# Optimization experiments

Measured on AMD Instinct MI355X. Metric: run time of the kernel, lower is better.

The kernel has to match this reference:

```python
import jax, jax.numpy as jnp
import numpy as np

N_SRC = 200_000
N_DST = 40_000
N_EDGES = 8_000_000
N_LAYERS = 6
TH_R = 0.4  # dR threshold for class_name == 'supercharged'


def delta_r(phi0, eta0, phi1, eta1):
    deta = eta0 - eta1
    dphi = phi0 - phi1
    pi = jnp.float32(np.pi)
    dphi = jnp.where(dphi > pi, dphi - 2 * pi, dphi)
    dphi = jnp.where(dphi < -pi, dphi + 2 * pi, dphi)
    return jnp.sqrt(deta ** 2 + dphi ** 2)


def setup_inputs() -> dict:
    key = jax.random.key(0)
    ks = jax.random.split(key, 8)
    src = jax.random.randint(ks[0], (N_EDGES,), 0, N_SRC, dtype=jnp.int32)
    dst = jax.random.randint(ks[1], (N_EDGES,), 0, N_DST, dtype=jnp.int32)
    energy = jax.random.uniform(ks[2], (N_SRC,), dtype=jnp.float32)
    layer = jax.random.randint(ks[3], (N_SRC,), 0, N_LAYERS, dtype=jnp.int32)
    eta_src = jax.random.normal(ks[4], (N_SRC,), dtype=jnp.float32)
    phi_src = jax.random.normal(ks[5], (N_SRC,), dtype=jnp.float32)
    eta_dst = jax.random.normal(ks[6], (N_DST,), dtype=jnp.float32)
    phi_dst = jax.random.normal(ks[7], (N_DST,), dtype=jnp.float32)
    return {"src": src, "dst": dst, "energy": energy, "layer": layer,
            "eta_src": eta_src, "phi_src": phi_src,
            "eta_dst": eta_dst, "phi_dst": phi_dst}


def reference(src, dst, energy, layer, eta_src, phi_src, eta_dst, phi_dst):
    # --- edge_function_dR_reco: per-edge gather + dR mask ---
    dR = delta_r(phi_src[src], eta_src[src], phi_dst[dst], eta_dst[dst])  # [E]
    edge_dR_labels = (dR < TH_R).astype(energy.dtype)                      # [E]

    # --- particle_message: 6 layer-bucketed masked energies per edge ---
    e = energy[src] * edge_dR_labels                                       # [E]
    onehot = (layer[src][:, None] == jnp.arange(N_LAYERS)[None, :])        # [E,6]
    msgs = e[:, None] * onehot.astype(e.dtype)                             # [E,6]

    # --- particle_update: ragged mailbox sum + sample std per dst node ---
    seg_sum = jax.ops.segment_sum(msgs, dst, num_segments=N_DST)           # [N_dst,6]
    seg_sq = jax.ops.segment_sum(msgs * msgs, dst, num_segments=N_DST)     # [N_dst,6]
    deg = jax.ops.segment_sum(jnp.ones_like(e), dst, num_segments=N_DST)   # [N_dst]
    deg = deg[:, None]

    valid = deg > 1
    mean = seg_sum / jnp.maximum(deg, 1.0)
    # unbiased sample variance, as in torch.std(dim=1)
    var = (seg_sq - deg * mean * mean) / jnp.maximum(deg - 1.0, 1.0)
    var = jnp.maximum(var, 0.0)
    safe = var > 0
    std = jnp.where(safe, jnp.sqrt(jnp.where(safe, var, 1.0)), 0.0)
    std = jnp.where(valid, std, 0.0)

    return jnp.concatenate([seg_sum, std], axis=1)  # [N_dst, 12]
```

## Files before the change

kernel.cpp:

```cpp
#include <hip/hip_runtime.h>
#include <math.h>

#define N_SRC 200000
#define N_DST 40000
#define N_EDGES 8000000
#define N_LAYERS 6

#define EBLK 256
#define ETPB 1024
#define PDST_LDS 12288

typedef int vint4 __attribute__((ext_vector_type(4)));

__device__ float4 g_psrc[N_SRC];
__device__ float2 g_pdst[N_DST];
__device__ unsigned int g_partial[EBLK][N_DST / 4];

__global__ __launch_bounds__(256) void pack_kernel(
        const float* __restrict__ energy, const int* __restrict__ layer,
        const float* __restrict__ eta_s, const float* __restrict__ phi_s,
        const float* __restrict__ eta_d, const float* __restrict__ phi_d) {
    int i = blockIdx.x * blockDim.x + threadIdx.x;
    if (i < N_SRC) {
        float4 p;
        p.x = energy[i];
        p.y = eta_s[i];
        p.z = phi_s[i];
        p.w = __int_as_float(layer[i]);
        g_psrc[i] = p;
    }
    if (i < N_DST) g_pdst[i] = make_float2(eta_d[i], phi_d[i]);
}

__device__ __forceinline__ void edge_compute(const float2* __restrict__ pcache,
                                             unsigned int* __restrict__ bins,
                                             int s, int d,
                                             float* __restrict__ out) {
    atomicAdd(&bins[d >> 2], 1u << ((d & 3) * 8));

    float4 p = g_psrc[s];
    float2 q;
    if (d < PDST_LDS) q = pcache[d];
    else              q = g_pdst[d];

    const float pif   = 3.14159265358979323846f;
    const float twopi = 6.28318530717958647692f;
    float deta = p.y - q.x;
    float dphi = p.z - q.y;
    dphi = (dphi >  pif) ? dphi - twopi : dphi;
    dphi = (dphi < -pif) ? dphi + twopi : dphi;
    float dr = sqrtf(deta * deta + dphi * dphi);
    if (dr < 0.4f) {
        int   l = __float_as_int(p.w);
        float e = p.x;
        float* base = out + (size_t)d * 12;
        atomicAdd(base + l,     e);
        atomicAdd(base + 6 + l, e * e);
    }
}

__global__ __launch_bounds__(ETPB) void edge_kernel(
        const vint4* __restrict__ src4, const vint4* __restrict__ dst4,
        float* __restrict__ out) {
    __shared__ unsigned int bins[N_DST / 4];
    __shared__ float2 pcache[PDST_LDS];

    for (int i = threadIdx.x; i < N_DST / 4; i += ETPB) bins[i] = 0u;
    for (int i = threadIdx.x; i < PDST_LDS; i += ETPB) pcache[i] = g_pdst[i];
    __syncthreads();

    const int nvec = N_EDGES / 4;
    for (int v = blockIdx.x * ETPB + threadIdx.x; v < nvec; v += EBLK * ETPB) {
        vint4 s4 = __builtin_nontemporal_load(src4 + v);
        vint4 d4 = __builtin_nontemporal_load(dst4 + v);
        edge_compute(pcache, bins, s4.x, d4.x, out);
        edge_compute(pcache, bins, s4.y, d4.y, out);
        edge_compute(pcache, bins, s4.z, d4.z, out);
        edge_compute(pcache, bins, s4.w, d4.w, out);
    }
    __syncthreads();

    unsigned int* po = &g_partial[blockIdx.x][0];
    for (int i = threadIdx.x; i < N_DST / 4; i += ETPB)
        __builtin_nontemporal_store(bins[i], po + i);
}

__device__ __forceinline__ void finalize_one(float* __restrict__ out, int d, float dg) {
    float mean_den = fmaxf(dg, 1.0f);
    float var_den  = fmaxf(dg - 1.0f, 1.0f);
    bool  valid    = dg > 1.0f;
    float* base = out + (size_t)d * 12;
#pragma unroll
    for (int l = 0; l < N_LAYERS; ++l) {
        float s = base[l];
        float q = base[6 + l];
        float mean = s / mean_den;
        float t = dg * mean;
        t = t * mean;
        float var = (q - t) / var_den;
        var = fmaxf(var, 0.0f);
        float sd = (var > 0.0f) ? sqrtf(var) : 0.0f;
        if (!valid) sd = 0.0f;
        base[6 + l] = sd;
    }
}

__global__ __launch_bounds__(256) void finalize_kernel(float* __restrict__ out) {
    int t = blockIdx.x * blockDim.x + threadIdx.x;
    if (t >= N_DST / 4) return;
    unsigned int c0 = 0, c1 = 0, c2 = 0, c3 = 0;
#pragma unroll 8
    for (int p = 0; p < EBLK; ++p) {
        unsigned int w = g_partial[p][t];
        c0 += w & 255u;
        c1 += (w >> 8) & 255u;
        c2 += (w >> 16) & 255u;
        c3 += (w >> 24);
    }
    finalize_one(out, 4 * t + 0, (float)c0);
    finalize_one(out, 4 * t + 1, (float)c1);
    finalize_one(out, 4 * t + 2, (float)c2);
    finalize_one(out, 4 * t + 3, (float)c3);
}

extern "C" void kernel_launch(void* const* d_in, const int* in_sizes, int n_in,
                              void* d_out, int out_size, void* d_ws, size_t ws_size,
                              hipStream_t stream) {
    const int*   src     = (const int*)  d_in[0];
    const int*   dst     = (const int*)  d_in[1];
    const float* energy  = (const float*)d_in[2];
    const int*   layer   = (const int*)  d_in[3];
    const float* eta_src = (const float*)d_in[4];
    const float* phi_src = (const float*)d_in[5];
    const float* eta_dst = (const float*)d_in[6];
    const float* phi_dst = (const float*)d_in[7];
    float* out = (float*)d_out;

    hipMemsetAsync(out, 0, (size_t)N_DST * 12 * sizeof(float), stream);

    pack_kernel<<<(N_SRC + 255) / 256, 256, 0, stream>>>(
        energy, layer, eta_src, phi_src, eta_dst, phi_dst);

    edge_kernel<<<EBLK, ETPB, 0, stream>>>(
        (const vint4*)src, (const vint4*)dst, out);

    finalize_kernel<<<(N_DST / 4 + 255) / 256, 256, 0, stream>>>(out);
}
```

Before: 214.0 us.

## Drop LDS dst cache, retune edge grid, fold output zeroing into pack kernel

Removes the 96KB shared-memory cache of destination eta/phi, so dst coordinates are gathered from global memory, where the 320KB table should sit in L2. This shrinks each edge block's LDS to the 40KB bin array. The edge grid moves to 512 blocks of 512 threads with a higher waves-per-EU launch bound, which allows several blocks to be resident per CU and raises occupancy for hiding gather and atomic latency. The output memset is merged into the pack kernel to save one launch. In exchange, every edge now does a global dst load, and finalize must reduce twice as many per-block count partials.

```diff
diff --git a/kernel.cpp b/kernel.cpp
--- a/kernel.cpp
+++ b/kernel.cpp
@@ -5,10 +5,10 @@
 #define N_DST 40000
 #define N_EDGES 8000000
 #define N_LAYERS 6
+#define N_OUT (N_DST * 12)
 
-#define EBLK 256
-#define ETPB 1024
-#define PDST_LDS 12288
+#define EBLK 512
+#define ETPB 512
 
 typedef int vint4 __attribute__((ext_vector_type(4)));
 
@@ -19,7 +19,8 @@
 __global__ __launch_bounds__(256) void pack_kernel(
         const float* __restrict__ energy, const int* __restrict__ layer,
         const float* __restrict__ eta_s, const float* __restrict__ phi_s,
-        const float* __restrict__ eta_d, const float* __restrict__ phi_d) {
+        const float* __restrict__ eta_d, const float* __restrict__ phi_d,
+        float* __restrict__ out) {
     int i = blockIdx.x * blockDim.x + threadIdx.x;
     if (i < N_SRC) {
         float4 p;
@@ -30,18 +31,16 @@
         g_psrc[i] = p;
     }
     if (i < N_DST) g_pdst[i] = make_float2(eta_d[i], phi_d[i]);
+    if (i < N_OUT) out[i] = 0.0f;
 }
 
-__device__ __forceinline__ void edge_compute(const float2* __restrict__ pcache,
-                                             unsigned int* __restrict__ bins,
+__device__ __forceinline__ void edge_compute(unsigned int* __restrict__ bins,
                                              int s, int d,
                                              float* __restrict__ out) {
     atomicAdd(&bins[d >> 2], 1u << ((d & 3) * 8));
 
     float4 p = g_psrc[s];
-    float2 q;
-    if (d < PDST_LDS) q = pcache[d];
-    else              q = g_pdst[d];
+    float2 q = g_pdst[d];
 
     const float pif   = 3.14159265358979323846f;
     const float twopi = 6.28318530717958647692f;
@@ -59,24 +58,22 @@
     }
 }
 
-__global__ __launch_bounds__(ETPB) void edge_kernel(
+__global__ __launch_bounds__(ETPB, 8) void edge_kernel(
         const vint4* __restrict__ src4, const vint4* __restrict__ dst4,
         float* __restrict__ out) {
     __shared__ unsigned int bins[N_DST / 4];
-    __shared__ float2 pcache[PDST_LDS];
 
     for (int i = threadIdx.x; i < N_DST / 4; i += ETPB) bins[i] = 0u;
-    for (int i = threadIdx.x; i < PDST_LDS; i += ETPB) pcache[i] = g_pdst[i];
     __syncthreads();
 
     const int nvec = N_EDGES / 4;
     for (int v = blockIdx.x * ETPB + threadIdx.x; v < nvec; v += EBLK * ETPB) {
         vint4 s4 = __builtin_nontemporal_load(src4 + v);
         vint4 d4 = __builtin_nontemporal_load(dst4 + v);
-        edge_compute(pcache, bins, s4.x, d4.x, out);
-        edge_compute(pcache, bins, s4.y, d4.y, out);
-        edge_compute(pcache, bins, s4.z, d4.z, out);
-        edge_compute(pcache, bins, s4.w, d4.w, out);
+        edge_compute(bins, s4.x, d4.x, out);
+        edge_compute(bins, s4.y, d4.y, out);
+        edge_compute(bins, s4.z, d4.z, out);
+        edge_compute(bins, s4.w, d4.w, out);
     }
     __syncthreads();
 
@@ -136,10 +133,8 @@
     const float* phi_dst = (const float*)d_in[7];
     float* out = (float*)d_out;
 
-    hipMemsetAsync(out, 0, (size_t)N_DST * 12 * sizeof(float), stream);
-
-    pack_kernel<<<(N_SRC + 255) / 256, 256, 0, stream>>>(
-        energy, layer, eta_src, phi_src, eta_dst, phi_dst);
+    pack_kernel<<<(N_OUT + 255) / 256, 256, 0, stream>>>(
+        energy, layer, eta_src, phi_src, eta_dst, phi_dst, out);
 
     edge_kernel<<<EBLK, ETPB, 0, stream>>>(
         (const vint4*)src, (const vint4*)dst, out);
```

After: 233.3 us. 1.09x slower.
